# Optimization experiments

Measured on AMD Instinct MI355X. Metric: run time of the kernel, lower is better.

Reference implementation:

```python
import jax, jax.numpy as jnp
from jax import lax
import numpy as np

B, T, V, E, H = 64, 256, 50000, 256, 512
HD = H // 2            # per-direction hidden
TAGS, START, STOP = 20, 18, 19


def setup_inputs() -> dict:
    key = jax.random.key(0)
    ks = jax.random.split(key, 18)
    s = 0.1  # param scale
    sentences = jax.random.randint(ks[0], (B, T), 0, V)
    emb = jax.random.normal(ks[1], (V, E), jnp.float32) * s
    Wih_f = jax.random.normal(ks[2], (4 * HD, E), jnp.float32) * s
    Whh_f = jax.random.normal(ks[3], (4 * HD, HD), jnp.float32) * s
    bih_f = jax.random.normal(ks[4], (4 * HD,), jnp.float32) * s
    bhh_f = jax.random.normal(ks[5], (4 * HD,), jnp.float32) * s
    Wih_b = jax.random.normal(ks[6], (4 * HD, E), jnp.float32) * s
    Whh_b = jax.random.normal(ks[7], (4 * HD, HD), jnp.float32) * s
    bih_b = jax.random.normal(ks[8], (4 * HD,), jnp.float32) * s
    bhh_b = jax.random.normal(ks[9], (4 * HD,), jnp.float32) * s
    Wl = jax.random.normal(ks[10], (TAGS, H), jnp.float32) * s
    bl = jax.random.normal(ks[11], (TAGS,), jnp.float32) * s
    trans = jax.random.normal(ks[12], (TAGS, TAGS), jnp.float32)
    trans = trans.at[:, START].set(-1000.0).at[STOP, :].set(-1000.0)
    # init_hidden(): uniform(-1, 1), shape [2*num_layer, B, HD] for h and c
    h0 = jax.random.uniform(ks[13], (2, B, HD), jnp.float32, -1.0, 1.0)
    c0 = jax.random.uniform(ks[14], (2, B, HD), jnp.float32, -1.0, 1.0)
    return dict(sentences=sentences, emb=emb, Wih_f=Wih_f, Whh_f=Whh_f,
                bih_f=bih_f, bhh_f=bhh_f, Wih_b=Wih_b, Whh_b=Whh_b,
                bih_b=bih_b, bhh_b=bhh_b, Wl=Wl, bl=bl, trans=trans,
                h0=h0, c0=c0)


def _lstm_dir(x_tbe, Wih, Whh, bih, bhh, h, c):
    # x_tbe: [T,B,E]; PyTorch gate order i,f,g,o
    gx = jnp.einsum('tbe,ge->tbg', x_tbe, Wih) + bih + bhh  # [T,B,4HD]
    def step(carry, gx_t):
        h, c = carry
        g = gx_t + h @ Whh.T
        i, f, gg, o = jnp.split(g, 4, axis=-1)
        c = jax.nn.sigmoid(f) * c + jax.nn.sigmoid(i) * jnp.tanh(gg)
        h = jax.nn.sigmoid(o) * jnp.tanh(c)
        return (h, c), h
    _, hs = lax.scan(step, (h, c), gx)
    return hs  # [T,B,HD]


def reference(sentences, emb, Wih_f, Whh_f, bih_f, bhh_f,
              Wih_b, Whh_b, bih_b, bhh_b, Wl, bl, trans, h0, c0):
    x = emb[sentences].transpose(1, 0, 2)             # [T,B,E]
    hf = _lstm_dir(x, Wih_f, Whh_f, bih_f, bhh_f, h0[0], c0[0])
    hb = _lstm_dir(x[::-1], Wih_b, Whh_b, bih_b, bhh_b, h0[1], c0[1])[::-1]
    out = jnp.concatenate([hf, hb], axis=-1)          # [T,B,H]
    logits = out @ Wl.T + bl                          # [T,B,TAGS]

    # Viterbi DP (all sentences at full length T, vectorized over batch)
    trellis0 = logits[0]                              # [B,TAGS]
    def vstep(prev, logit_t):
        v = prev[:, :, None] + trans[None]            # [B, prev_tag, cur_tag]
        new = logit_t + v.max(axis=1)
        return new, (new, v.argmax(axis=1))
    _, (trellis_rest, bps) = lax.scan(vstep, trellis0, logits[1:])
    trellis = jnp.concatenate([trellis0[None], trellis_rest], 0)  # [T,B,TAGS]

    last_tag = jnp.argmax(trellis[-1], axis=-1)       # [B]
    def bstep(tag, bp):                               # bp: [B,TAGS]
        prev = jnp.take_along_axis(bp, tag[:, None], axis=1)[:, 0]
        return prev, prev
    _, path_rev = lax.scan(bstep, last_tag, bps[::-1])
    path = jnp.concatenate([path_rev[::-1], last_tag[None]], 0)  # [T,B]

    probs = jnp.take_along_axis(jax.nn.softmax(trellis, axis=-1),
                                path[:, :, None], axis=2)[:, :, 0]  # [T,B]
    scores = trellis[-1].max(axis=-1)                 # [B]
    return scores, path.T, probs.T
```

## Files before the change

### kernel.cpp

```cpp
#include <hip/hip_runtime.h>

typedef unsigned int uint;
typedef unsigned short ushort;
typedef __attribute__((ext_vector_type(4))) float f4;
typedef __attribute__((ext_vector_type(8))) short bf8;

#define T_ 256
#define B_ 64
#define E_ 256
#define HD_ 256
#define NTAG 20

#define GX_OFF 0ull
#define LG_OFF 33554432ull
#define FLG_OFF 33882112ull
#define Q_OFFF 33884160ull

#define WHHF_HI 0u
#define WHHB_HI 524288u
#define WIHF_HI 1048576u
#define WIHB_HI 1572864u
#define LO_D    262144u
#define WL_HI   2097152u
#define WL_LO   2107392u
#define HS_HI   2117632u
#define HS_LO   10539008u
#define HS_DIR  4210688ull

__device__ __forceinline__ ushort f2bf(float x){
  uint u = __float_as_uint(x);
  uint r = (u + 0x7fffu + ((u >> 16) & 1u)) >> 16;
  return (ushort)r;
}
__device__ __forceinline__ float bf2f(ushort h){ return __uint_as_float(((uint)h) << 16); }
__device__ __forceinline__ void splitf(float x, ushort &h, ushort &l){
  h = f2bf(x);
  l = f2bf(x - bf2f(h));
}
__device__ __forceinline__ f4 mfma16(bf8 a, bf8 b, f4 c){
  return __builtin_amdgcn_mfma_f32_16x16x32_bf16(a, b, c, 0, 0, 0);
}
__device__ __forceinline__ float sigm(float x){ return 1.0f / (1.0f + expf(-x)); }

#define LD16(dst, base, off) \
  asm volatile("global_load_dwordx4 %0, %1, off offset:" #off " sc0 sc1" \
               : "=v"(dst) : "v"(base))
#define ST2(base, off, val) \
  asm volatile("global_store_short %0, %1, off offset:" #off " sc0 sc1" \
               :: "v"(base), "v"(val) : "memory")

__global__ void k0_split(const float* __restrict__ whhF, const float* __restrict__ whhB,
                         const float* __restrict__ wihF, const float* __restrict__ wihB,
                         const float* __restrict__ wl, const float* __restrict__ h0,
                         ushort* __restrict__ q, uint* __restrict__ flags){
  uint stride = gridDim.x * blockDim.x;
  for (uint i = blockIdx.x * blockDim.x + threadIdx.x; i < 1093632u; i += stride){
    float x; uint hbase;
    if (i < 262144u){ x = whhF[i]; hbase = WHHF_HI + i; }
    else if (i < 524288u){ x = whhB[i - 262144u]; hbase = WHHB_HI + (i - 262144u); }
    else if (i < 786432u){ x = wihF[i - 524288u]; hbase = WIHF_HI + (i - 524288u); }
    else if (i < 1048576u){ x = wihB[i - 786432u]; hbase = WIHB_HI + (i - 786432u); }
    else if (i < 1058816u){
      uint j = i - 1048576u;
      ushort h, l; splitf(wl[j], h, l);
      q[WL_HI + j] = h; q[WL_LO + j] = l;
      continue;
    } else if (i < 1091584u){
      uint j = i - 1058816u;
      uint dir = j >> 14, rem = j & 16383u;
      ushort h, l; splitf(h0[j], h, l);
      q[HS_HI + dir * (uint)HS_DIR + rem] = h;
      q[HS_LO + dir * (uint)HS_DIR + rem] = l;
      continue;
    } else {
      __hip_atomic_store(&flags[i - 1091584u], 0u, __ATOMIC_RELAXED,
                         __HIP_MEMORY_SCOPE_AGENT);
      continue;
    }
    ushort h, l; splitf(x, h, l);
    q[hbase] = h; q[hbase + LO_D] = l;
  }
}

__global__ __launch_bounds__(256) void k1_gx(const int* __restrict__ sents,
    const float* __restrict__ emb, const ushort* __restrict__ q,
    const float* __restrict__ bihF, const float* __restrict__ bhhF,
    const float* __restrict__ bihB, const float* __restrict__ bhhB,
    float* __restrict__ gx)
{
  __shared__ ushort Bs[2][64][256];
  const int tid = threadIdx.x;
  const int dir = blockIdx.z;
  const int n0 = blockIdx.x * 64;
  const int r0 = blockIdx.y * 64;
  const ushort* whi = q + (dir ? WIHB_HI : WIHF_HI);

  for (int cid = tid; cid < 4096; cid += 256){
    int half = cid >> 11;
    int c = (cid >> 5) & 63;
    int kc = cid & 31;
    const ushort* src = whi + half * LO_D + (size_t)(n0 + c) * 256 + kc * 8;
    uint4 v = *(const uint4*)src;
    *(uint4*)&Bs[half][c][(kc ^ (c & 31)) * 8] = v;
  }
  __syncthreads();

  const int w = tid >> 6, l = tid & 63;
  const int lrow = l & 15, lk8 = (l >> 4) * 8;
  const int r = r0 + w * 16 + lrow;
  const int t = r >> 6, b = r & 63;
  const int tok = sents[b * T_ + (dir ? (T_ - 1 - t) : t)];
  const float* arow = emb + (size_t)tok * E_;

  f4 acc[4];
  #pragma unroll
  for (int i = 0; i < 4; i++){ acc[i][0]=0.f; acc[i][1]=0.f; acc[i][2]=0.f; acc[i][3]=0.f; }

  for (int ks = 0; ks < 8; ks++){
    const float* ap = arow + ks * 32 + lk8;
    f4 v0 = *(const f4*)ap;
    f4 v1 = *(const f4*)(ap + 4);
    bf8 ah, al;
    #pragma unroll
    for (int j = 0; j < 4; j++){
      ushort hh, ll;
      splitf(v0[j], hh, ll); ah[j] = (short)hh; al[j] = (short)ll;
      splitf(v1[j], hh, ll); ah[4 + j] = (short)hh; al[4 + j] = (short)ll;
    }
    const int kc = ks * 4 + (l >> 4);
    #pragma unroll
    for (int nt = 0; nt < 4; nt++){
      const int c = nt * 16 + lrow;
      const int skc = kc ^ (c & 31);
      bf8 bh = *(const bf8*)&Bs[0][c][skc * 8];
      bf8 blo = *(const bf8*)&Bs[1][c][skc * 8];
      acc[nt] = mfma16(ah, bh, acc[nt]);
      acc[nt] = mfma16(ah, blo, acc[nt]);
      acc[nt] = mfma16(al, bh, acc[nt]);
    }
  }

  const float* bih = dir ? bihB : bihF;
  const float* bhh = dir ? bhhB : bhhF;
  #pragma unroll
  for (int nt = 0; nt < 4; nt++){
    int col = n0 + nt * 16 + lrow;
    float bias = bih[col] + bhh[col];
    int gate = col >> 8, un = col & 255;
    size_t plane = (size_t)(dir * 16 + (un >> 4));
    int u15 = un & 15;
    #pragma unroll
    for (int reg = 0; reg < 4; reg++){
      int row = r0 + w * 16 + (l >> 4) * 4 + reg;
      int tt = row >> 6, bb = row & 63;
      gx[((plane * 256 + tt) * 64 + bb) * 64 + gate * 16 + u15] = acc[nt][reg] + bias;
    }
  }
}

__global__ __launch_bounds__(256) void k2_persist(const ushort* __restrict__ q,
    const float* __restrict__ gx, const float* __restrict__ c0,
    ushort* __restrict__ hsHi, ushort* __restrict__ hsLo, uint* __restrict__ flags)
{
  __shared__ ushort Bs[2][64][256];
  const int tid = threadIdx.x;
  const int bid = blockIdx.x;
  const int dir = bid >> 4;
  const int ub = bid & 15;
  const int u0 = ub * 16;
  const ushort* whi = q + (dir ? WHHB_HI : WHHF_HI);

  for (int cid = tid; cid < 4096; cid += 256){
    int half = cid >> 11;
    int c = (cid >> 5) & 63;
    int kc = cid & 31;
    int grow = (c >> 4) * 256 + u0 + (c & 15);
    const ushort* src = whi + half * LO_D + (size_t)grow * 256 + kc * 8;
    uint4 v = *(const uint4*)src;
    *(uint4*)&Bs[half][c][(kc ^ (c & 31)) * 8] = v;
  }
  __syncthreads();

  const int w = tid >> 6, l = tid & 63;
  const int lrow = l & 15, lk8 = (l >> 4) * 8;
  const int arow = w * 16 + lrow;
  const int unit = u0 + lrow;
  const int erow = w * 16 + (l >> 4) * 4;

  float creg[4];
  #pragma unroll
  for (int reg = 0; reg < 4; reg++)
    creg[reg] = c0[dir * 16384 + (erow + reg) * 256 + unit];

  const float* gxp = gx + (size_t)(dir * 16 + ub) * (256ull * 4096ull);
  ushort* hHiD = hsHi + (size_t)dir * HS_DIR;
  ushort* hLoD = hsLo + (size_t)dir * HS_DIR;
  uint* fb = flags + dir * 1024;

  for (int t = 0; t < T_; t++){
    float gv[4][4];
    #pragma unroll
    for (int reg = 0; reg < 4; reg++)
      #pragma unroll
      for (int gate = 0; gate < 4; gate++)
        gv[reg][gate] = gxp[((size_t)t * 64 + (erow + reg)) * 64 + gate * 16 + lrow];

    const ushort* rowHi = hHiD + (size_t)t * 16384 + arow * 256 + lk8;
    const ushort* rowLo = hLoD + (size_t)t * 16384 + arow * 256 + lk8;
    bf8 ah[8], al[8];
    LD16(ah[0], rowHi, 0);   LD16(al[0], rowLo, 0);
    LD16(ah[1], rowHi, 64);  LD16(al[1], rowLo, 64);
    LD16(ah[2], rowHi, 128); LD16(al[2], rowLo, 128);
    LD16(ah[3], rowHi, 192); LD16(al[3], rowLo, 192);
    LD16(ah[4], rowHi, 256); LD16(al[4], rowLo, 256);
    LD16(ah[5], rowHi, 320); LD16(al[5], rowLo, 320);
    LD16(ah[6], rowHi, 384); LD16(al[6], rowLo, 384);
    LD16(ah[7], rowHi, 448); LD16(al[7], rowLo, 448);
    asm volatile("s_waitcnt vmcnt(0)" ::: "memory");
    __builtin_amdgcn_sched_barrier(0);

    f4 acc[4];
    #pragma unroll
    for (int i = 0; i < 4; i++){ acc[i][0]=0.f; acc[i][1]=0.f; acc[i][2]=0.f; acc[i][3]=0.f; }

    #pragma unroll
    for (int ks = 0; ks < 8; ks++){
      const int kc = ks * 4 + (l >> 4);
      #pragma unroll
      for (int nt = 0; nt < 4; nt++){
        const int c = nt * 16 + lrow;
        const int skc = kc ^ (c & 31);
        bf8 bh  = *(const bf8*)&Bs[0][c][skc * 8];
        bf8 blo = *(const bf8*)&Bs[1][c][skc * 8];
        acc[nt] = mfma16(ah[ks], bh, acc[nt]);
        acc[nt] = mfma16(ah[ks], blo, acc[nt]);
        acc[nt] = mfma16(al[ks], bh, acc[nt]);
      }
    }

    ushort* oHi = hHiD + (size_t)(t + 1) * 16384 + erow * 256 + unit;
    ushort* oLo = hLoD + (size_t)(t + 1) * 16384 + erow * 256 + unit;
    ushort hh_[4], ll_[4];
    #pragma unroll
    for (int reg = 0; reg < 4; reg++){
      float g0 = acc[0][reg] + gv[reg][0];
      float g1 = acc[1][reg] + gv[reg][1];
      float g2 = acc[2][reg] + gv[reg][2];
      float g3 = acc[3][reg] + gv[reg][3];
      float cn = sigm(g1) * creg[reg] + sigm(g0) * tanhf(g2);
      float hn = sigm(g3) * tanhf(cn);
      creg[reg] = cn;
      splitf(hn, hh_[reg], ll_[reg]);
    }
    ST2(oHi, 0, hh_[0]);    ST2(oLo, 0, ll_[0]);
    ST2(oHi, 512, hh_[1]);  ST2(oLo, 512, ll_[1]);
    ST2(oHi, 1024, hh_[2]); ST2(oLo, 1024, ll_[2]);
    ST2(oHi, 1536, hh_[3]); ST2(oLo, 1536, ll_[3]);

    if (t + 1 < T_){
      asm volatile("s_waitcnt vmcnt(0)" ::: "memory");
      __syncthreads();
      if (tid == 0)
        __hip_atomic_store(&fb[ub * 16], (uint)(t + 1), __ATOMIC_RELAXED,
                           __HIP_MEMORY_SCOPE_AGENT);
      if (w == 0){
        uint e = (uint)(t + 1);
        uint fv;
        do {
          fv = (l < 16) ? __hip_atomic_load(&fb[(l & 15) * 16], __ATOMIC_RELAXED,
                                            __HIP_MEMORY_SCOPE_AGENT)
                        : 0xffffffffu;
        } while (!__all(fv >= e));
      }
      __syncthreads();
      __builtin_amdgcn_sched_barrier(0);
    }
  }
}

__global__ __launch_bounds__(256) void k3_logits(const ushort* __restrict__ q,
    const float* __restrict__ bl, float* __restrict__ logits)
{
  __shared__ ushort Bs[2][32][512];
  const int tid = threadIdx.x;
  const int r0 = blockIdx.x * 64;
  const ushort* hsHi = q + HS_HI;
  const ushort* hsLo = q + HS_LO;

  for (int cid = tid; cid < 4096; cid += 256){
    int half = cid >> 11;
    int c = (cid >> 6) & 31;
    int kc = cid & 63;
    uint4 v; v.x = 0; v.y = 0; v.z = 0; v.w = 0;
    if (c < NTAG){
      const ushort* src = q + (half ? WL_LO : WL_HI) + (size_t)c * 512 + kc * 8;
      v = *(const uint4*)src;
    }
    *(uint4*)&Bs[half][c][(kc ^ (c & 31)) * 8] = v;
  }
  __syncthreads();

  const int w = tid >> 6, l = tid & 63;
  const int lrow = l & 15, lk8 = (l >> 4) * 8;
  const int r = r0 + w * 16 + lrow;
  const int t = r >> 6, b = r & 63;

  f4 acc[2];
  #pragma unroll
  for (int i = 0; i < 2; i++){ acc[i][0]=0.f; acc[i][1]=0.f; acc[i][2]=0.f; acc[i][3]=0.f; }

  for (int ks = 0; ks < 16; ks++){
    int k = ks * 32 + lk8;
    size_t off;
    if (k < 256)
      off = (size_t)(t + 1) * 16384 + (size_t)b * 256 + k;
    else
      off = HS_DIR + (size_t)(256 - t) * 16384 + (size_t)b * 256 + (k - 256);
    bf8 ah = *(const bf8*)&hsHi[off];
    bf8 al = *(const bf8*)&hsLo[off];
    int kc = k >> 3;
    #pragma unroll
    for (int nt = 0; nt < 2; nt++){
      int c = nt * 16 + lrow;
      int skc = kc ^ (c & 31);
      bf8 bh  = *(const bf8*)&Bs[0][c][skc * 8];
      bf8 blo = *(const bf8*)&Bs[1][c][skc * 8];
      acc[nt] = mfma16(ah, bh, acc[nt]);
      acc[nt] = mfma16(ah, blo, acc[nt]);
      acc[nt] = mfma16(al, bh, acc[nt]);
    }
  }

  #pragma unroll
  for (int nt = 0; nt < 2; nt++){
    int tag = nt * 16 + lrow;
    if (tag < NTAG){
      float bias = bl[tag];
      #pragma unroll
      for (int reg = 0; reg < 4; reg++){
        int row = r0 + w * 16 + (l >> 4) * 4 + reg;
        logits[(size_t)row * NTAG + tag] = acc[nt][reg] + bias;
      }
    }
  }
}

__global__ __launch_bounds__(64) void k4_viterbi(const float* __restrict__ logits,
    const float* __restrict__ trans, float* __restrict__ out)
{
  const int b = blockIdx.x, tid = threadIdx.x;
  __shared__ float tr[NTAG][NTAG];
  __shared__ float trell[T_][NTAG];
  __shared__ unsigned char bp[T_][NTAG];
  __shared__ int path[T_];
  __shared__ float cur[NTAG], nv[NTAG];

  for (int i = tid; i < NTAG * NTAG; i += 64) tr[i / NTAG][i % NTAG] = trans[i];
  if (tid < NTAG){
    float v = logits[(size_t)b * NTAG + tid];
    cur[tid] = v; trell[0][tid] = v;
  }
  __syncthreads();

  for (int t = 1; t < T_; t++){
    if (tid < NTAG){
      float best = -3.0e38f; int bi = 0;
      #pragma unroll
      for (int p = 0; p < NTAG; p++){
        float v = cur[p] + tr[p][tid];
        if (v > best){ best = v; bi = p; }
      }
      float nvv = logits[((size_t)t * 64 + b) * NTAG + tid] + best;
      nv[tid] = nvv; trell[t][tid] = nvv; bp[t][tid] = (unsigned char)bi;
    }
    __syncthreads();
    if (tid < NTAG) cur[tid] = nv[tid];
    __syncthreads();
  }

  if (tid == 0){
    float best = -3.0e38f; int bi = 0;
    for (int c = 0; c < NTAG; c++){
      if (trell[T_ - 1][c] > best){ best = trell[T_ - 1][c]; bi = c; }
    }
    out[b] = best;
    path[T_ - 1] = bi;
    for (int t = T_ - 1; t >= 1; t--) path[t - 1] = bp[t][path[t]];
  }
  __syncthreads();

  for (int t = tid; t < T_; t += 64){
    float m = -3.0e38f;
    for (int c = 0; c < NTAG; c++) m = fmaxf(m, trell[t][c]);
    float s = 0.f;
    for (int c = 0; c < NTAG; c++) s += expf(trell[t][c] - m);
    float p = expf(trell[t][path[t]] - m) / s;
    out[64 + (size_t)b * T_ + t] = (float)path[t];
    out[64 + 64 * T_ + (size_t)b * T_ + t] = p;
  }
}

extern "C" void kernel_launch(void* const* d_in, const int* in_sizes, int n_in,
                              void* d_out, int out_size, void* d_ws, size_t ws_size,
                              hipStream_t stream){
  (void)in_sizes; (void)n_in; (void)out_size; (void)ws_size;
  const int*   sents = (const int*)d_in[0];
  const float* emb   = (const float*)d_in[1];
  const float* wihF  = (const float*)d_in[2];
  const float* whhF  = (const float*)d_in[3];
  const float* bihF  = (const float*)d_in[4];
  const float* bhhF  = (const float*)d_in[5];
  const float* wihB  = (const float*)d_in[6];
  const float* whhB  = (const float*)d_in[7];
  const float* bihB  = (const float*)d_in[8];
  const float* bhhB  = (const float*)d_in[9];
  const float* wl    = (const float*)d_in[10];
  const float* bl    = (const float*)d_in[11];
  const float* trans = (const float*)d_in[12];
  const float* h0    = (const float*)d_in[13];
  const float* c0    = (const float*)d_in[14];

  float* wsf    = (float*)d_ws;
  ushort* q     = (ushort*)(wsf + Q_OFFF);
  float* gx     = wsf + GX_OFF;
  float* logits = wsf + LG_OFF;
  uint* flags   = (uint*)(wsf + FLG_OFF);
  float* out    = (float*)d_out;
  ushort* hsHi  = q + HS_HI;
  ushort* hsLo  = q + HS_LO;

  k0_split<<<1024, 256, 0, stream>>>(whhF, whhB, wihF, wihB, wl, h0, q, flags);
  k1_gx<<<dim3(16, 256, 2), 256, 0, stream>>>(sents, emb, q, bihF, bhhF, bihB, bhhB, gx);

  {
    const ushort* qa = q; const float* gxa = gx; const float* c0a = c0;
    ushort* hia = hsHi; ushort* loa = hsLo; uint* fla = flags;
    void* args[] = { (void*)&qa, (void*)&gxa, (void*)&c0a,
                     (void*)&hia, (void*)&loa, (void*)&fla };
    hipLaunchCooperativeKernel((const void*)k2_persist, dim3(32), dim3(256),
                               args, 0, stream);
  }

  k3_logits<<<256, 256, 0, stream>>>(q, bl, logits);
  k4_viterbi<<<64, 64, 0, stream>>>(logits, trans, out);
}
```

Measured before the change: 1.724 ms.

## Pin recurrent LSTM workgroups to one XCC and prefetch gate inputs

The persistent recurrent kernel now launches 256 workgroups. Each reads its XCC id and takes a ticket, and only the first XCC to gather 32 workgroups keeps them; the rest exit. This keeps inter-workgroup flag syncs and h exchanges inside one XCC's L2, so loads and stores can use sc0 instead of system-coherent sc0 sc1. It also re-lays gx so each thread loads its gate inputs as contiguous float4s, double-buffered two steps ahead. The h loads for the next step are issued right after the barrier. The spin-wait gains an iteration guard, and the election relies on at least 32 workgroups landing on one XCC, which could fail or misbehave silently.

After: 1.588 ms. 1.09x faster.

```diff
diff --git a/kernel.cpp b/kernel.cpp
--- a/kernel.cpp
+++ b/kernel.cpp
@@ -27,6 +27,9 @@
 #define HS_LO   10539008u
 #define HS_DIR  4210688ull
 
+#define ECTL_CNT 512u
+#define ECTL_LDR 520u
+
 __device__ __forceinline__ ushort f2bf(float x){
   uint u = __float_as_uint(x);
   uint r = (u + 0x7fffu + ((u >> 16) & 1u)) >> 16;
@@ -42,12 +45,17 @@
 }
 __device__ __forceinline__ float sigm(float x){ return 1.0f / (1.0f + expf(-x)); }
 
-#define LD16(dst, base, off) \
-  asm volatile("global_load_dwordx4 %0, %1, off offset:" #off " sc0 sc1" \
+#define LDH(dst, base, off) \
+  asm volatile("global_load_dwordx4 %0, %1, off offset:" #off " sc0" \
+               : "=v"(dst) : "v"(base))
+#define LDG16(dst, base, off) \
+  asm volatile("global_load_dwordx4 %0, %1, off offset:" #off \
                : "=v"(dst) : "v"(base))
 #define ST2(base, off, val) \
-  asm volatile("global_store_short %0, %1, off offset:" #off " sc0 sc1" \
+  asm volatile("global_store_short %0, %1, off offset:" #off " sc0" \
                :: "v"(base), "v"(val) : "memory")
+#define STFLAG(p, v) \
+  asm volatile("global_store_dword %0, %1, off sc0" :: "v"(p), "v"(v) : "memory")
 
 __global__ void k0_split(const float* __restrict__ whhF, const float* __restrict__ whhB,
                          const float* __restrict__ wihF, const float* __restrict__ wihB,
@@ -73,8 +81,9 @@
       q[HS_LO + dir * (uint)HS_DIR + rem] = l;
       continue;
     } else {
-      __hip_atomic_store(&flags[i - 1091584u], 0u, __ATOMIC_RELAXED,
-                         __HIP_MEMORY_SCOPE_AGENT);
+      uint j = i - 1091584u;
+      __hip_atomic_store(&flags[j], (j == ECTL_LDR) ? 0xffffffffu : 0u,
+                         __ATOMIC_RELAXED, __HIP_MEMORY_SCOPE_AGENT);
       continue;
     }
     ushort h, l; splitf(x, h, l);
@@ -146,28 +155,121 @@
   for (int nt = 0; nt < 4; nt++){
     int col = n0 + nt * 16 + lrow;
     float bias = bih[col] + bhh[col];
-    int gate = col >> 8, un = col & 255;
-    size_t plane = (size_t)(dir * 16 + (un >> 4));
-    int u15 = un & 15;
+    int gate = col >> 8, ug = (col >> 4) & 15;
     #pragma unroll
     for (int reg = 0; reg < 4; reg++){
       int row = r0 + w * 16 + (l >> 4) * 4 + reg;
-      int tt = row >> 6, bb = row & 63;
-      gx[((plane * 256 + tt) * 64 + bb) * 64 + gate * 16 + u15] = acc[nt][reg] + bias;
-    }
-  }
-}
-
-__global__ __launch_bounds__(256) void k2_persist(const ushort* __restrict__ q,
+      int tt = row >> 6, b2 = row & 63;
+      int ctid = ((b2 >> 4) << 6) | (((b2 >> 2) & 3) << 4) | lrow;
+      gx[(((size_t)(dir * 16 + ug) * 256 + tt) * 256 + ctid) * 16
+         + (b2 & 3) * 4 + gate] = acc[nt][reg] + bias;
+    }
+  }
+}
+
+
+#define K2_STEP(TT, GC)                                                             \
+{                                                                                   \
+  const int t_ = (TT);                                                              \
+  asm volatile("s_waitcnt vmcnt(4)" ::: "memory");                                  \
+  __builtin_amdgcn_sched_barrier(0);                                                \
+  f4 acc[4];                                                                        \
+  _Pragma("unroll")                                                                 \
+  for (int i = 0; i < 4; i++){ acc[i][0]=0.f; acc[i][1]=0.f; acc[i][2]=0.f; acc[i][3]=0.f; } \
+  _Pragma("unroll")                                                                 \
+  for (int ks = 0; ks < 8; ks++){                                                   \
+    const int kc = ks * 4 + (l >> 4);                                               \
+    _Pragma("unroll")                                                               \
+    for (int nt = 0; nt < 4; nt++){                                                 \
+      const int c = nt * 16 + lrow;                                                 \
+      const int skc = kc ^ (c & 31);                                                \
+      bf8 bh  = *(const bf8*)&Bs[0][c][skc * 8];                                    \
+      bf8 blo = *(const bf8*)&Bs[1][c][skc * 8];                                    \
+      acc[nt] = mfma16(ah[ks], bh, acc[nt]);                                        \
+      acc[nt] = mfma16(ah[ks], blo, acc[nt]);                                       \
+      acc[nt] = mfma16(al[ks], bh, acc[nt]);                                        \
+    }                                                                               \
+  }                                                                                 \
+  {                                                                                 \
+    ushort* oHi = hHiD + (size_t)(t_ + 1) * 16384 + erow * 256 + unit;              \
+    ushort* oLo = hLoD + (size_t)(t_ + 1) * 16384 + erow * 256 + unit;              \
+    ushort hh_[4], ll_[4];                                                          \
+    _Pragma("unroll")                                                               \
+    for (int reg = 0; reg < 4; reg++){                                              \
+      float g0 = acc[0][reg] + GC[reg][0];                                          \
+      float g1 = acc[1][reg] + GC[reg][1];                                          \
+      float g2 = acc[2][reg] + GC[reg][2];                                          \
+      float g3 = acc[3][reg] + GC[reg][3];                                          \
+      float cn = sigm(g1) * creg[reg] + sigm(g0) * tanhf(g2);                       \
+      float hn = sigm(g3) * tanhf(cn);                                              \
+      creg[reg] = cn;                                                               \
+      splitf(hn, hh_[reg], ll_[reg]);                                               \
+    }                                                                               \
+    ST2(oHi, 0, hh_[0]);    ST2(oLo, 0, ll_[0]);                                    \
+    ST2(oHi, 512, hh_[1]);  ST2(oLo, 512, ll_[1]);                                  \
+    ST2(oHi, 1024, hh_[2]); ST2(oLo, 1024, ll_[2]);                                 \
+    ST2(oHi, 1536, hh_[3]); ST2(oLo, 1536, ll_[3]);                                 \
+  }                                                                                 \
+  if (t_ + 1 < T_){                                                                 \
+    asm volatile("s_waitcnt vmcnt(0)" ::: "memory");                                \
+    __builtin_amdgcn_sched_barrier(0);                                              \
+    __syncthreads();                                                                \
+    uint e = (uint)(t_ + 1);                                                        \
+    if (tid == 0) STFLAG(fb + (ub << 4), e);                                        \
+    if (w == 0){                                                                    \
+      uint fv = 0xffffffffu;                                                        \
+      const uint* fp = fb + ((l & 15) << 4);                                        \
+      int guard = 0;                                                                \
+      do {                                                                          \
+        if (l < 16) asm volatile("global_load_dword %0, %1, off sc0"                \
+                                 : "=v"(fv) : "v"(fp));                             \
+        asm volatile("s_waitcnt vmcnt(0)" ::: "memory");                            \
+      } while (!__all(fv >= e) && ++guard < 16384);                                 \
+    }                                                                               \
+    __syncthreads();                                                                \
+    __builtin_amdgcn_sched_barrier(0);                                              \
+    const ushort* rh = hHiD + (size_t)(t_ + 1) * 16384 + arow * 256 + lk8;          \
+    const ushort* rl = hLoD + (size_t)(t_ + 1) * 16384 + arow * 256 + lk8;          \
+    LDH(ah[0], rh, 0);   LDH(ah[1], rh, 64);  LDH(ah[2], rh, 128); LDH(ah[3], rh, 192); \
+    LDH(ah[4], rh, 256); LDH(ah[5], rh, 320); LDH(ah[6], rh, 384); LDH(ah[7], rh, 448); \
+    LDH(al[0], rl, 0);   LDH(al[1], rl, 64);  LDH(al[2], rl, 128); LDH(al[3], rl, 192); \
+    LDH(al[4], rl, 256); LDH(al[5], rl, 320); LDH(al[6], rl, 384); LDH(al[7], rl, 448); \
+    int t2 = (t_ + 2 < T_) ? (t_ + 2) : (T_ - 1);                                   \
+    const float* pn = gxp + ((size_t)t2 * 256 + tid) * 16;                          \
+    LDG16(GC[0], pn, 0); LDG16(GC[1], pn, 16);                                      \
+    LDG16(GC[2], pn, 32); LDG16(GC[3], pn, 48);                                     \
+  }                                                                                 \
+}
+
+__global__ __launch_bounds__(256, 1) void k2_persist(const ushort* __restrict__ q,
     const float* __restrict__ gx, const float* __restrict__ c0,
     ushort* __restrict__ hsHi, ushort* __restrict__ hsLo, uint* __restrict__ flags)
 {
   __shared__ ushort Bs[2][64][256];
+  __shared__ int s_tk;
   const int tid = threadIdx.x;
-  const int bid = blockIdx.x;
-  const int dir = bid >> 4;
-  const int ub = bid & 15;
-  const int u0 = ub * 16;
+
+  if (tid == 0){
+    uint xcc;
+    asm volatile("s_getreg_b32 %0, hwreg(HW_REG_XCC_ID)" : "=s"(xcc));
+    xcc &= 7u;
+    uint my = atomicAdd(&flags[ECTL_CNT + xcc], 1u);
+    if (my == 31u) atomicCAS(&flags[ECTL_LDR], 0xffffffffu, xcc);
+    uint L = 0xffffffffu;
+    for (int g = 0; g < (1 << 20); ++g){
+      L = __hip_atomic_load(&flags[ECTL_LDR], __ATOMIC_RELAXED,
+                            __HIP_MEMORY_SCOPE_AGENT);
+      if (L != 0xffffffffu) break;
+    }
+    s_tk = (L == xcc && my < 32u) ? (int)my : -1;
+  }
+  __syncthreads();
+  const int ticket = s_tk;
+  if (ticket < 0) return;
+
+  const int dir = ticket >> 4;
+  const int ub  = ticket & 15;
+  const int u0  = ub * 16;
   const ushort* whi = q + (dir ? WHHB_HI : WHHF_HI);
 
   for (int cid = tid; cid < 4096; cid += 256){
@@ -191,91 +293,35 @@
   #pragma unroll
   for (int reg = 0; reg < 4; reg++)
     creg[reg] = c0[dir * 16384 + (erow + reg) * 256 + unit];
-
-  const float* gxp = gx + (size_t)(dir * 16 + ub) * (256ull * 4096ull);
+  asm volatile("" :: "v"(creg[0]), "v"(creg[1]), "v"(creg[2]), "v"(creg[3]));
+
   ushort* hHiD = hsHi + (size_t)dir * HS_DIR;
   ushort* hLoD = hsLo + (size_t)dir * HS_DIR;
+  const float* gxp = gx + (size_t)(dir * 16 + ub) * 1048576ull;
   uint* fb = flags + dir * 1024;
 
-  for (int t = 0; t < T_; t++){
-    float gv[4][4];
-    #pragma unroll
-    for (int reg = 0; reg < 4; reg++)
-      #pragma unroll
-      for (int gate = 0; gate < 4; gate++)
-        gv[reg][gate] = gxp[((size_t)t * 64 + (erow + reg)) * 64 + gate * 16 + lrow];
-
-    const ushort* rowHi = hHiD + (size_t)t * 16384 + arow * 256 + lk8;
-    const ushort* rowLo = hLoD + (size_t)t * 16384 + arow * 256 + lk8;
-    bf8 ah[8], al[8];
-    LD16(ah[0], rowHi, 0);   LD16(al[0], rowLo, 0);
-    LD16(ah[1], rowHi, 64);  LD16(al[1], rowLo, 64);
-    LD16(ah[2], rowHi, 128); LD16(al[2], rowLo, 128);
-    LD16(ah[3], rowHi, 192); LD16(al[3], rowLo, 192);
-    LD16(ah[4], rowHi, 256); LD16(al[4], rowLo, 256);
-    LD16(ah[5], rowHi, 320); LD16(al[5], rowLo, 320);
-    LD16(ah[6], rowHi, 384); LD16(al[6], rowLo, 384);
-    LD16(ah[7], rowHi, 448); LD16(al[7], rowLo, 448);
-    asm volatile("s_waitcnt vmcnt(0)" ::: "memory");
-    __builtin_amdgcn_sched_barrier(0);
-
-    f4 acc[4];
-    #pragma unroll
-    for (int i = 0; i < 4; i++){ acc[i][0]=0.f; acc[i][1]=0.f; acc[i][2]=0.f; acc[i][3]=0.f; }
-
-    #pragma unroll
-    for (int ks = 0; ks < 8; ks++){
-      const int kc = ks * 4 + (l >> 4);
-      #pragma unroll
-      for (int nt = 0; nt < 4; nt++){
-        const int c = nt * 16 + lrow;
-        const int skc = kc ^ (c & 31);
-        bf8 bh  = *(const bf8*)&Bs[0][c][skc * 8];
-        bf8 blo = *(const bf8*)&Bs[1][c][skc * 8];
-        acc[nt] = mfma16(ah[ks], bh, acc[nt]);
-        acc[nt] = mfma16(ah[ks], blo, acc[nt]);
-        acc[nt] = mfma16(al[ks], bh, acc[nt]);
-      }
-    }
-
-    ushort* oHi = hHiD + (size_t)(t + 1) * 16384 + erow * 256 + unit;
-    ushort* oLo = hLoD + (size_t)(t + 1) * 16384 + erow * 256 + unit;
-    ushort hh_[4], ll_[4];
-    #pragma unroll
-    for (int reg = 0; reg < 4; reg++){
-      float g0 = acc[0][reg] + gv[reg][0];
-      float g1 = acc[1][reg] + gv[reg][1];
-      float g2 = acc[2][reg] + gv[reg][2];
-      float g3 = acc[3][reg] + gv[reg][3];
-      float cn = sigm(g1) * creg[reg] + sigm(g0) * tanhf(g2);
-      float hn = sigm(g3) * tanhf(cn);
-      creg[reg] = cn;
-      splitf(hn, hh_[reg], ll_[reg]);
-    }
-    ST2(oHi, 0, hh_[0]);    ST2(oLo, 0, ll_[0]);
-    ST2(oHi, 512, hh_[1]);  ST2(oLo, 512, ll_[1]);
-    ST2(oHi, 1024, hh_[2]); ST2(oLo, 1024, ll_[2]);
-    ST2(oHi, 1536, hh_[3]); ST2(oLo, 1536, ll_[3]);
-
-    if (t + 1 < T_){
-      asm volatile("s_waitcnt vmcnt(0)" ::: "memory");
-      __syncthreads();
-      if (tid == 0)
-        __hip_atomic_store(&fb[ub * 16], (uint)(t + 1), __ATOMIC_RELAXED,
-                           __HIP_MEMORY_SCOPE_AGENT);
-      if (w == 0){
-        uint e = (uint)(t + 1);
-        uint fv;
-        do {
-          fv = (l < 16) ? __hip_atomic_load(&fb[(l & 15) * 16], __ATOMIC_RELAXED,
-                                            __HIP_MEMORY_SCOPE_AGENT)
-                        : 0xffffffffu;
-        } while (!__all(fv >= e));
-      }
-      __syncthreads();
-      __builtin_amdgcn_sched_barrier(0);
-    }
-  }
+  f4 ga[4], gb[4];
+  bf8 ah[8], al[8];
+
+  {
+    const float* p0 = gxp + (size_t)tid * 16;
+    LDG16(ga[0], p0, 0); LDG16(ga[1], p0, 16); LDG16(ga[2], p0, 32); LDG16(ga[3], p0, 48);
+    const ushort* rh = hHiD + arow * 256 + lk8;
+    const ushort* rl = hLoD + arow * 256 + lk8;
+    LDH(ah[0], rh, 0);   LDH(ah[1], rh, 64);  LDH(ah[2], rh, 128); LDH(ah[3], rh, 192);
+    LDH(ah[4], rh, 256); LDH(ah[5], rh, 320); LDH(ah[6], rh, 384); LDH(ah[7], rh, 448);
+    LDH(al[0], rl, 0);   LDH(al[1], rl, 64);  LDH(al[2], rl, 128); LDH(al[3], rl, 192);
+    LDH(al[4], rl, 256); LDH(al[5], rl, 320); LDH(al[6], rl, 384); LDH(al[7], rl, 448);
+    const float* p1 = gxp + ((size_t)256 + tid) * 16;
+    LDG16(gb[0], p1, 0); LDG16(gb[1], p1, 16); LDG16(gb[2], p1, 32); LDG16(gb[3], p1, 48);
+  }
+
+  #pragma unroll 1
+  for (int t = 0; t < T_; t += 2){
+    K2_STEP(t, ga);
+    K2_STEP(t + 1, gb);
+  }
+  asm volatile("s_waitcnt vmcnt(0)" ::: "memory");
 }
 
 __global__ __launch_bounds__(256) void k3_logits(const ushort* __restrict__ q,
@@ -437,7 +483,7 @@
     ushort* hia = hsHi; ushort* loa = hsLo; uint* fla = flags;
     void* args[] = { (void*)&qa, (void*)&gxa, (void*)&c0a,
                      (void*)&hia, (void*)&loa, (void*)&fla };
-    hipLaunchCooperativeKernel((const void*)k2_persist, dim3(32), dim3(256),
+    hipLaunchCooperativeKernel((const void*)k2_persist, dim3(256), dim3(256),
                                args, 0, stream);
   }
 
```
